# Optimization experiments

Measured on AMD Instinct MI355X. Metric: run time of the kernel, lower is better.

The kernel has to match this reference:

```python
import jax, jax.numpy as jnp
import numpy as np

B, S, D = 2, 2048, 4096
H, KVH, DH = 32, 8, 128
KVD = KVH * DH  # 1024
EPS = 1e-6
SCALING = DH ** -0.5


def _rms_norm(x, scale):
    xf = x.astype(jnp.float32)
    var = jnp.mean(xf * xf, axis=-1, keepdims=True)
    return (xf * jax.lax.rsqrt(var + EPS)).astype(x.dtype) * scale


def _rotate_half(x):
    half = x.shape[-1] // 2
    return jnp.concatenate([-x[..., half:], x[..., :half]], axis=-1)


def setup_inputs() -> dict:
    key = jax.random.key(0)
    ks = jax.random.split(key, 5)
    hidden_states = jax.random.normal(ks[0], (B, S, D), dtype=jnp.float32)
    w_qkv = jax.random.normal(ks[1], (D, D + 2 * KVD), dtype=jnp.float32) * 0.02
    w_out = jax.random.normal(ks[2], (D, D), dtype=jnp.float32) * 0.02
    q_scale = jnp.ones((D,), dtype=jnp.float32)
    k_scale = jnp.ones((KVD,), dtype=jnp.float32)
    # real rotary tables: cos/sin of positions, broadcast to batch
    inv_freq = 1.0 / (10000.0 ** (np.arange(0, DH, 2, dtype=np.float32) / DH))
    pos = np.arange(S, dtype=np.float32)
    freqs = np.outer(pos, inv_freq)            # [S, DH/2]
    emb = np.concatenate([freqs, freqs], -1)   # [S, DH]
    cos_cached = jnp.broadcast_to(jnp.asarray(np.cos(emb)), (B, S, DH))
    sin_cached = jnp.broadcast_to(jnp.asarray(np.sin(emb)), (B, S, DH))
    # causal mask: True = masked
    idx = jnp.arange(S)
    attention_mask = (idx[None, :] > idx[:, None])[None, None].repeat(B, 0)  # [B,1,S,S] bool
    return {
        "hidden_states": hidden_states, "w_qkv": w_qkv, "w_out": w_out,
        "q_scale": q_scale, "k_scale": k_scale,
        "cos_cached": cos_cached, "sin_cached": sin_cached,
        "attention_mask": attention_mask,
    }


def reference(hidden_states, w_qkv, w_out, q_scale, k_scale, cos_cached, sin_cached, attention_mask):
    b, s, _ = hidden_states.shape
    qkv = jnp.einsum("bsd,de->bse", hidden_states, w_qkv)
    q, k, v = jnp.split(qkv, [D, D + KVD], axis=-1)
    # qk-norm applied pre-view over full projected dim (non-qwen3 path)
    q = _rms_norm(q, q_scale)
    k = _rms_norm(k, k_scale)
    q = q.reshape(b, s, H, DH).transpose(0, 2, 1, 3)    # [B,H,S,DH]
    k = k.reshape(b, s, KVH, DH).transpose(0, 2, 1, 3)  # [B,KVH,S,DH]
    v = v.reshape(b, s, KVH, DH).transpose(0, 2, 1, 3)
    cos = cos_cached[:, None]  # [B,1,S,DH]
    sin = sin_cached[:, None]
    q = q * cos + _rotate_half(q) * sin
    k = k * cos + _rotate_half(k) * sin
    # repeat KV heads to match query heads (GQA)
    n_rep = H // KVH
    k = jnp.repeat(k, n_rep, axis=1)
    v = jnp.repeat(v, n_rep, axis=1)
    scores = jnp.einsum("bhsd,bhtd->bhst", q, k) * SCALING
    scores = jnp.where(attention_mask, jnp.float32(-10000.0), scores)
    attn = jax.nn.softmax(scores.astype(jnp.float32), axis=-1).astype(q.dtype)
    out = jnp.einsum("bhst,bhtd->bhsd", attn, v)
    out = out.transpose(0, 2, 1, 3).reshape(b, s, H * DH)
    return jnp.einsum("bsd,de->bse", out, w_out)
```

## Files before the change

kernel.cpp:

```cpp
#include <hip/hip_runtime.h>
#include <hip/hip_bf16.h>
#include <cstdint>
#include <cstddef>

#define BB 2
#define SS 2048
#define DD 4096
#define HH 32
#define KVH 8
#define DH 128
#define KVD 1024
#define SCALE 0.08838834764831845f
#define QSC 0.1275178745225f

typedef __attribute__((ext_vector_type(8))) short short8;
typedef __attribute__((ext_vector_type(4))) float f32x4;

typedef __attribute__((address_space(1))) void GV;
typedef __attribute__((address_space(3))) void LV;

__device__ __forceinline__ void async16(const void* g, void* l) {
  __builtin_amdgcn_global_load_lds((GV*)g, (LV*)l, 16, 0, 0);
}

__device__ __forceinline__ unsigned short f2bf(float x) {
  union { float f; uint32_t u; } v; v.f = x;
  uint32_t r = (v.u + 0x7fffu + ((v.u >> 16) & 1u)) >> 16;
  return (unsigned short)r;
}
__device__ __forceinline__ float bf2f(unsigned short b) {
  union { uint32_t u; float f; } v; v.u = ((uint32_t)b) << 16; return v.f;
}
__device__ __forceinline__ f32x4 mfma16(short8 a, short8 b, f32x4 c) {
  return __builtin_amdgcn_mfma_f32_16x16x32_bf16(a, b, c, 0, 0, 0);
}

__global__ __launch_bounds__(256) void cast_bf16_kernel(
    const float* __restrict__ in, unsigned short* __restrict__ out, int n4) {
  int i = blockIdx.x * 256 + threadIdx.x;
  if (i >= n4) return;
  float4 v = ((const float4*)in)[i];
  ushort4 o;
  o.x = f2bf(v.x); o.y = f2bf(v.y); o.z = f2bf(v.z); o.w = f2bf(v.w);
  ((ushort4*)out)[i] = o;
}

__global__ __launch_bounds__(256) void transpose_cast_kernel(
    const float* __restrict__ in, unsigned short* __restrict__ out, int R, int C) {
  __shared__ unsigned short tile[32][33];
  const int tx = threadIdx.x, ty = threadIdx.y;
  const int c0 = blockIdx.x * 32, r0 = blockIdx.y * 32;
  for (int i = ty; i < 32; i += 8)
    tile[i][tx] = f2bf(in[(size_t)(r0 + i) * C + c0 + tx]);
  __syncthreads();
  for (int i = ty; i < 32; i += 8)
    out[(size_t)(c0 + i) * R + r0 + tx] = tile[tx][i];
}

__global__ __launch_bounds__(256) void transpose_v_kernel(
    const unsigned short* __restrict__ qkv, unsigned short* __restrict__ vo) {
  __shared__ unsigned short tile[32][33];
  const int s0 = blockIdx.x * 32, d0 = blockIdx.y * 32;
  const int b = blockIdx.z >> 3, kvh = blockIdx.z & 7;
  const int tx = threadIdx.x, ty = threadIdx.y;
  const unsigned short* ip = qkv + 5120 + (size_t)kvh * 128 + d0 + tx;
  for (int i = ty; i < 32; i += 8)
    tile[i][tx] = ip[(size_t)(b * SS + s0 + i) * 6144];
  __syncthreads();
  unsigned short* op = vo + (size_t)(b * KVH + kvh) * DH * SS + s0 + tx;
  for (int i = ty; i < 32; i += 8)
    op[(size_t)(d0 + i) * SS] = tile[tx][i];
}

template <typename OutT>
__global__ __launch_bounds__(256, 2) void gemm_bt(
    const unsigned short* __restrict__ A, const unsigned short* __restrict__ Bt,
    OutT* __restrict__ C, int M, int N, int K) {
  __shared__ __align__(16) unsigned short As[4096];
  __shared__ __align__(16) unsigned short Bs[4096];
  const int tid = threadIdx.x;
  const int wave = tid >> 6, lane = tid & 63, quad = lane >> 4, l16 = lane & 15;
  const int m0 = blockIdx.x * 128, n0 = blockIdx.y * 128;
  const int wm = (wave & 1) * 64, wn = (wave >> 1) * 64;
  f32x4 acc[4][4] = {};
  const int sr = tid >> 2;
  const int sg = (tid & 3) ^ ((tid >> 3) & 3);
  const unsigned short* Ag = A + (size_t)(m0 + sr) * K + sg * 8;
  const unsigned short* Bg = Bt + (size_t)(n0 + sr) * K + sg * 8;
  unsigned short* AsW = As + wave * 512;
  unsigned short* BsW = Bs + wave * 512;
  const int pg = (quad ^ ((l16 >> 1) & 3)) * 8;
  for (int k0 = 0; k0 < K; k0 += 32) {
    __syncthreads();
    async16(Ag + k0, AsW);
    async16(Ag + (size_t)64 * K + k0, AsW + 2048);
    async16(Bg + k0, BsW);
    async16(Bg + (size_t)64 * K + k0, BsW + 2048);
    __syncthreads();
    short8 af[4], bf[4];
#pragma unroll
    for (int i = 0; i < 4; i++) {
      af[i] = *(const short8*)&As[(wm + i * 16 + l16) * 32 + pg];
      bf[i] = *(const short8*)&Bs[(wn + i * 16 + l16) * 32 + pg];
    }
#pragma unroll
    for (int mi = 0; mi < 4; mi++)
#pragma unroll
      for (int ni = 0; ni < 4; ni++)
        acc[mi][ni] = mfma16(af[mi], bf[ni], acc[mi][ni]);
  }
#pragma unroll
  for (int mi = 0; mi < 4; mi++)
#pragma unroll
    for (int ni = 0; ni < 4; ni++)
#pragma unroll
      for (int r = 0; r < 4; r++) {
        int row = m0 + wm + mi * 16 + quad * 4 + r;
        int col = n0 + wn + ni * 16 + l16;
        float v = acc[mi][ni][r];
        if constexpr (sizeof(OutT) == 4) C[(size_t)row * N + col] = v;
        else                             C[(size_t)row * N + col] = (OutT)f2bf(v);
      }
}

__global__ __launch_bounds__(256) void rmsnorm_rope_kernel(
    const unsigned short* __restrict__ qkv,
    const float* __restrict__ q_scale, const float* __restrict__ k_scale,
    const float* __restrict__ cosc, const float* __restrict__ sinc,
    unsigned short* __restrict__ qo,
    unsigned short* __restrict__ ko)
{
  const int row = blockIdx.x;
  const int b = row >> 11, s = row & 2047;
  const int tid = threadIdx.x;
  const unsigned short* qr = qkv + (size_t)row * 6144;
  short8 qv0 = *(const short8*)&qr[tid * 8];
  short8 qv1 = *(const short8*)&qr[2048 + tid * 8];
  ushort4 kv = *(const ushort4*)&qr[4096 + tid * 4];
  float sq = 0.f, sk = 0.f;
#pragma unroll
  for (int e = 0; e < 8; e++) {
    float a = bf2f((unsigned short)qv0[e]); sq += a * a;
    float c = bf2f((unsigned short)qv1[e]); sq += c * c;
  }
  float kf[4];
#pragma unroll
  for (int e = 0; e < 4; e++) {
    kf[e] = bf2f(((const unsigned short*)&kv)[e]); sk += kf[e] * kf[e];
  }
#pragma unroll
  for (int off = 32; off; off >>= 1) {
    sq += __shfl_down(sq, off, 64);
    sk += __shfl_down(sk, off, 64);
  }
  __shared__ float redq[4], redk[4];
  if ((tid & 63) == 0) { redq[tid >> 6] = sq; redk[tid >> 6] = sk; }
  __syncthreads();
  sq = redq[0] + redq[1] + redq[2] + redq[3];
  sk = redk[0] + redk[1] + redk[2] + redk[3];
  const float rq = rsqrtf(sq * (1.f / 4096.f) + 1e-6f);
  const float rk = rsqrtf(sk * (1.f / 1024.f) + 1e-6f);
  const float* cp = cosc + (size_t)row * 128;
  const float* sp = sinc + (size_t)row * 128;
#pragma unroll
  for (int it = 0; it < 2; it++) {
    const int c = it * 2048 + tid * 8;
    const int d = c & 127, hh = c >> 7;
    short8 v8 = it ? qv1 : qv0;
    short8 p8 = *(const short8*)&qr[c ^ 64];
    const float sgn = (d < 64) ? -1.f : 1.f;
    ushort o8[8];
#pragma unroll
    for (int e = 0; e < 8; e++) {
      float v = bf2f((unsigned short)v8[e]) * rq * q_scale[c + e];
      float p = bf2f((unsigned short)p8[e]) * rq * q_scale[(c ^ 64) + e];
      o8[e] = f2bf((v * cp[d + e] + sgn * p * sp[d + e]) * QSC);
    }
    *(uint4*)&qo[((size_t)(b * HH + hh) * SS + s) * DH + d] = *(const uint4*)o8;
  }
  {
    const int c = tid * 4;
    const int d = c & 127, hh = c >> 7;
    ushort4 p4 = *(const ushort4*)&qr[4096 + (c ^ 64)];
    const float sgn = (d < 64) ? -1.f : 1.f;
    ushort o4[4];
#pragma unroll
    for (int e = 0; e < 4; e++) {
      float v = kf[e] * rk * k_scale[c + e];
      float p = bf2f(((const unsigned short*)&p4)[e]) * rk * k_scale[(c ^ 64) + e];
      o4[e] = f2bf(v * cp[d + e] + sgn * p * sp[d + e]);
    }
    *(uint2*)&ko[((size_t)(b * KVH + hh) * SS + s) * DH + d] = *(const uint2*)o4;
  }
}

__global__ __launch_bounds__(256, 2) void flash_attn(
    const unsigned short* __restrict__ Q,
    const unsigned short* __restrict__ Kr,
    const unsigned short* __restrict__ Vt,
    unsigned short* __restrict__ O)
{
  __shared__ __align__(16) unsigned short Ks[8192];
  __shared__ __align__(16) unsigned short Vs[8192];
  __shared__ __align__(16) unsigned int   Ps[4][1024];
  const int tid = threadIdx.x, wave = tid >> 6, lane = tid & 63;
  const int quad = lane >> 4, l16 = lane & 15;
  const int bh = blockIdx.x, b = bh >> 5, h = bh & 31;
  const int kvh = h >> 2;
  const int qbase = ((int)gridDim.y - 1 - (int)blockIdx.y) * 128;
  const unsigned short* Qb = Q + (size_t)(b * HH + h) * SS * DH;
  short8 qf[2][4];
#pragma unroll
  for (int mi = 0; mi < 2; mi++) {
    const unsigned short* Qp = Qb + (size_t)(qbase + mi * 64 + wave * 16 + l16) * DH + quad * 8;
#pragma unroll
    for (int c = 0; c < 4; c++) qf[mi][c] = *(const short8*)(Qp + c * 32);
  }
  const unsigned short* Kg = Kr + (size_t)(b * KVH + kvh) * SS * DH;
  const unsigned short* Vg = Vt + (size_t)(b * KVH + kvh) * DH * SS;
  int bK[4], bV[4];
#pragma unroll
  for (int j = 0; j < 4; j++) {
    const int kk = wave * 16 + j * 4 + quad;
    const int gd = l16 ^ ((j * 4 + quad) & 15);
    bK[j] = kk * 128 + gd * 8;
    const int dd = (wave * 4 + j) * 8 + (lane >> 3);
    const int gk = (lane & 7) ^ ((lane >> 3) & 7);
    bV[j] = dd * 2048 + gk * 8;
  }
  f32x4 o[2][8] = {};
  float m_i[2] = {-1e30f, -1e30f}, l_i[2] = {0.f, 0.f};
  const int ndiag = qbase >> 6;
  const int nkt = ndiag + 2;
  for (int kt = 0; kt < nkt; kt++) {
    const int k0 = kt * 64;
    __syncthreads();
#pragma unroll
    for (int j = 0; j < 4; j++) {
      async16(Kg + (size_t)k0 * 128 + bK[j], Ks + (wave * 4 + j) * 512);
      async16(Vg + k0 + bV[j], Vs + (wave * 4 + j) * 512);
    }
    __syncthreads();
    f32x4 st[4][2] = {};
#pragma unroll
    for (int km = 0; km < 4; km++) {
      const unsigned short* krow = Ks + (km * 16 + l16) * 128;
#pragma unroll
      for (int c = 0; c < 4; c++) {
        short8 kf = *(const short8*)(krow + (((c * 4 + quad) ^ l16) * 8));
        st[km][0] = mfma16(kf, qf[0][c], st[km][0]);
        st[km][1] = mfma16(kf, qf[1][c], st[km][1]);
      }
    }
    const bool mtile = (kt >= ndiag);
    float alpha[2];
#pragma unroll
    for (int mi = 0; mi < 2; mi++) {
      if (mtile) {
        const int qg = qbase + mi * 64 + wave * 16 + l16;
#pragma unroll
        for (int km = 0; km < 4; km++)
#pragma unroll
          for (int r = 0; r < 4; r++)
            if (k0 + km * 16 + quad * 4 + r > qg) st[km][mi][r] = -1e4f;
      }
      float tmax = -3e38f;
#pragma unroll
      for (int km = 0; km < 4; km++)
#pragma unroll
        for (int r = 0; r < 4; r++) tmax = fmaxf(tmax, st[km][mi][r]);
      tmax = fmaxf(tmax, __shfl_xor(tmax, 16, 64));
      tmax = fmaxf(tmax, __shfl_xor(tmax, 32, 64));
      const float mn = fmaxf(m_i[mi], tmax);
      alpha[mi] = __builtin_amdgcn_exp2f(m_i[mi] - mn);
      m_i[mi] = mn;
      float rs = 0.f;
#pragma unroll
      for (int km = 0; km < 4; km++)
#pragma unroll
        for (int r = 0; r < 4; r++) {
          float e = __builtin_amdgcn_exp2f(st[km][mi][r] - mn);
          st[km][mi][r] = e;
          rs += e;
        }
      rs += __shfl_xor(rs, 16, 64);
      rs += __shfl_xor(rs, 32, 64);
      l_i[mi] = l_i[mi] * alpha[mi] + rs;
      unsigned int* pw = &Ps[wave][(mi * 16 + l16) * 32 + (quad & 1) * 2];
#pragma unroll
      for (int km = 0; km < 4; km++) {
        const int g = (km * 2 + (quad >> 1)) ^ (l16 & 7);
        float e0 = st[km][mi][0], e1 = st[km][mi][1], e2 = st[km][mi][2], e3 = st[km][mi][3];
        pw[g * 4]     = __builtin_amdgcn_perm(__builtin_bit_cast(unsigned int, e1),
                                              __builtin_bit_cast(unsigned int, e0), 0x07060302u);
        pw[g * 4 + 1] = __builtin_amdgcn_perm(__builtin_bit_cast(unsigned int, e3),
                                              __builtin_bit_cast(unsigned int, e2), 0x07060302u);
      }
    }
    if (__any((alpha[0] != 1.f) || (alpha[1] != 1.f))) {
#pragma unroll
      for (int mi = 0; mi < 2; mi++) {
        float ar[4];
#pragma unroll
        for (int r = 0; r < 4; r++)
          ar[r] = __shfl(alpha[mi], (lane & 48) + quad * 4 + r, 64);
#pragma unroll
        for (int f = 0; f < 8; f++)
#pragma unroll
          for (int r = 0; r < 4; r++) o[mi][f][r] *= ar[r];
      }
    }
#pragma unroll
    for (int kc = 0; kc < 2; kc++) {
      short8 pa[2];
#pragma unroll
      for (int mi = 0; mi < 2; mi++) {
        const int g = (kc * 4 + quad) ^ (l16 & 7);
        uint4 pv4 = *(const uint4*)&Ps[wave][(mi * 16 + l16) * 32 + g * 4];
        pa[mi] = __builtin_bit_cast(short8, pv4);
      }
#pragma unroll
      for (int f = 0; f < 8; f++) {
        const int d = f * 16 + l16;
        short8 vf = *(const short8*)(Vs + d * 64 + (((kc * 4 + quad) ^ (l16 & 7)) * 8));
        o[0][f] = mfma16(pa[0], vf, o[0][f]);
        o[1][f] = mfma16(pa[1], vf, o[1][f]);
      }
    }
  }
  float il[2][4];
#pragma unroll
  for (int mi = 0; mi < 2; mi++)
#pragma unroll
    for (int r = 0; r < 4; r++) {
      float lv = __shfl(l_i[mi], (lane & 48) + quad * 4 + r, 64);
      il[mi][r] = 1.f / lv;
    }
#pragma unroll
  for (int mi = 0; mi < 2; mi++) {
    unsigned short* Op = O + (size_t)(b * SS + qbase + mi * 64 + wave * 16 + quad * 4) * DD + h * DH + l16;
#pragma unroll
    for (int f = 0; f < 8; f++)
#pragma unroll
      for (int r = 0; r < 4; r++)
        Op[(size_t)r * DD + f * 16] = f2bf(o[mi][f][r] * il[mi][r]);
  }
}

extern "C" void kernel_launch(void* const* d_in, const int* in_sizes, int n_in,
                              void* d_out, int out_size, void* d_ws, size_t ws_size,
                              hipStream_t stream) {
  const float* hs      = (const float*)d_in[0];
  const float* wqkv    = (const float*)d_in[1];
  const float* wout    = (const float*)d_in[2];
  const float* q_scale = (const float*)d_in[3];
  const float* k_scale = (const float*)d_in[4];
  const float* cosc    = (const float*)d_in[5];
  const float* sinc    = (const float*)d_in[6];
  float* out = (float*)d_out;

  unsigned short* ws = (unsigned short*)d_ws;
  unsigned short* wqkvT = ws;
  unsigned short* woutT = wqkvT + 25165824;
  unsigned short* hsb   = woutT + 16777216;
  unsigned short* qkv   = hsb + 16777216;
  unsigned short* qrope = wqkvT;
  unsigned short* krope = wqkvT + 16777216;
  unsigned short* vT    = wqkvT + 16777216 + 4194304;
  unsigned short* attno = hsb;

  cast_bf16_kernel<<<16384, 256, 0, stream>>>(hs, hsb, 4194304);
  transpose_cast_kernel<<<dim3(192, 128), dim3(32, 8), 0, stream>>>(wqkv, wqkvT, 4096, 6144);
  transpose_cast_kernel<<<dim3(128, 128), dim3(32, 8), 0, stream>>>(wout, woutT, 4096, 4096);
  gemm_bt<unsigned short><<<dim3(32, 48), 256, 0, stream>>>(hsb, wqkvT, qkv, 4096, 6144, 4096);
  rmsnorm_rope_kernel<<<4096, 256, 0, stream>>>(qkv, q_scale, k_scale, cosc, sinc,
                                                qrope, krope);
  transpose_v_kernel<<<dim3(64, 4, 16), dim3(32, 8), 0, stream>>>(qkv, vT);
  flash_attn<<<dim3(64, 16), 256, 0, stream>>>(qrope, krope, vT, attno);
  gemm_bt<float><<<dim3(32, 32), 256, 0, stream>>>(attno, woutT, out, 4096, 4096, 4096);
}
```

Baseline: 800.2 us.

## Rewrite bf16 GEMM as 256x256 double-buffered ping-pong kernel with XCD-aware tile mapping

Replaces the 128x128, single-buffered GEMM (256 threads, K-step 32) with a 512-thread 256x256 tile kernel that uses K-step 64. It double-buffers LDS with async global-to-LDS loads issued two tiles ahead and splits each iteration into four MFMA phases separated by barriers and setprio hints. Block indices are remapped so consecutive tiles land on the same XCD for L2 reuse, and the LDS layout uses an XOR swizzle. The goal is to raise MFMA utilisation and hide global latency in both projection GEMMs. The cost is 128KB of LDS per block and a large accumulator register footprint. The 256-wide tiles also leave fewer blocks (384 and 256) to fill the CUs.

```diff
diff --git a/kernel.cpp b/kernel.cpp
--- a/kernel.cpp
+++ b/kernel.cpp
@@ -72,56 +72,180 @@
     op[(size_t)(d0 + i) * SS] = tile[tx][i];
 }
 
+
+#define GBAR()  asm volatile("s_barrier" ::: "memory")
+#define GLGKM0()                                              \
+  do {                                                        \
+    asm volatile("s_waitcnt lgkmcnt(0)" ::: "memory");        \
+    __builtin_amdgcn_sched_barrier(0);                        \
+  } while (0)
+
+#define STG_A(tt, mh, p)                                                         \
+  do {                                                                           \
+    async16(Abase + (size_t)(arb0 + (mh) * 64) * K + (size_t)(tt) * 64 + loffA,  \
+            ldsA + (p) * 16384 + (arb0 + (mh) * 64) * 64);                       \
+    async16(Abase + (size_t)(arb1 + (mh) * 64) * K + (size_t)(tt) * 64 + loffA,  \
+            ldsA + (p) * 16384 + (arb1 + (mh) * 64) * 64);                       \
+  } while (0)
+#define STG_B(tt, nh, p)                                                         \
+  do {                                                                           \
+    async16(Bbase + (size_t)(brb0 + (nh) * 32) * K + (size_t)(tt) * 64 + loffB,  \
+            ldsB + (p) * 16384 + (brb0 + (nh) * 32) * 64);                       \
+    async16(Bbase + (size_t)(brb1 + (nh) * 32) * K + (size_t)(tt) * 64 + loffB,  \
+            ldsB + (p) * 16384 + (brb1 + (nh) * 32) * 64);                       \
+  } while (0)
+
 template <typename OutT>
-__global__ __launch_bounds__(256, 2) void gemm_bt(
+__global__ __launch_bounds__(512, 2) void gemm_bt(
     const unsigned short* __restrict__ A, const unsigned short* __restrict__ Bt,
     OutT* __restrict__ C, int M, int N, int K) {
-  __shared__ __align__(16) unsigned short As[4096];
-  __shared__ __align__(16) unsigned short Bs[4096];
+  __shared__ __align__(16) unsigned short lds[65536];
+  unsigned short* ldsA = lds;
+  unsigned short* ldsB = lds + 32768;
   const int tid = threadIdx.x;
-  const int wave = tid >> 6, lane = tid & 63, quad = lane >> 4, l16 = lane & 15;
-  const int m0 = blockIdx.x * 128, n0 = blockIdx.y * 128;
-  const int wm = (wave & 1) * 64, wn = (wave >> 1) * 64;
-  f32x4 acc[4][4] = {};
-  const int sr = tid >> 2;
-  const int sg = (tid & 3) ^ ((tid >> 3) & 3);
-  const unsigned short* Ag = A + (size_t)(m0 + sr) * K + sg * 8;
-  const unsigned short* Bg = Bt + (size_t)(n0 + sr) * K + sg * 8;
-  unsigned short* AsW = As + wave * 512;
-  unsigned short* BsW = Bs + wave * 512;
-  const int pg = (quad ^ ((l16 >> 1) & 3)) * 8;
-  for (int k0 = 0; k0 < K; k0 += 32) {
-    __syncthreads();
-    async16(Ag + k0, AsW);
-    async16(Ag + (size_t)64 * K + k0, AsW + 2048);
-    async16(Bg + k0, BsW);
-    async16(Bg + (size_t)64 * K + k0, BsW + 2048);
-    __syncthreads();
-    short8 af[4], bf[4];
-#pragma unroll
-    for (int i = 0; i < 4; i++) {
-      af[i] = *(const short8*)&As[(wm + i * 16 + l16) * 32 + pg];
-      bf[i] = *(const short8*)&Bs[(wn + i * 16 + l16) * 32 + pg];
-    }
-#pragma unroll
-    for (int mi = 0; mi < 4; mi++)
-#pragma unroll
-      for (int ni = 0; ni < 4; ni++)
-        acc[mi][ni] = mfma16(af[mi], bf[ni], acc[mi][ni]);
-  }
-#pragma unroll
-  for (int mi = 0; mi < 4; mi++)
-#pragma unroll
-    for (int ni = 0; ni < 4; ni++)
-#pragma unroll
-      for (int r = 0; r < 4; r++) {
-        int row = m0 + wm + mi * 16 + quad * 4 + r;
-        int col = n0 + wn + ni * 16 + l16;
-        float v = acc[mi][ni][r];
-        if constexpr (sizeof(OutT) == 4) C[(size_t)row * N + col] = v;
-        else                             C[(size_t)row * N + col] = (OutT)f2bf(v);
-      }
-}
+  const int wave = __builtin_amdgcn_readfirstlane(tid >> 6);
+  const int lane = tid & 63, quad = lane >> 4, l16 = lane & 15;
+
+  const int tn_n = N >> 8;
+  const int nwg = (int)gridDim.x;
+  const int q = nwg >> 3, r = nwg & 7;
+  const int xcd = (int)blockIdx.x & 7, lin = (int)blockIdx.x >> 3;
+  const int wg = (xcd < r) ? xcd * (q + 1) + lin
+                           : r * (q + 1) + (xcd - r) * q + lin;
+  const int m0 = (wg / tn_n) * 256, n0 = (wg % tn_n) * 256;
+
+  const int blk0 = wave * 2, blk1 = blk0 + 1;
+  const int arb0 = ((blk0 & 7) << 3) + ((blk0 >> 3) << 7);
+  const int arb1 = ((blk1 & 7) << 3) + ((blk1 >> 3) << 7);
+  const int brb0 = ((blk0 >> 2) << 6) + ((blk0 & 3) << 3);
+  const int brb1 = ((blk1 >> 2) << 6) + ((blk1 & 3) << 3);
+  const int lrow = lane >> 3;
+  const int loffA = lrow * K + (((lane & 7) ^ lrow) << 3);
+  const int loffB = loffA;
+  const unsigned short* Abase = A + (size_t)m0 * K;
+  const unsigned short* Bbase = Bt + (size_t)n0 * K;
+
+  const int pg0 = ((quad) ^ (l16 & 7)) * 8;
+  const int pg1 = ((quad + 4) ^ (l16 & 7)) * 8;
+  const int arow = ((wave >> 2) * 128 + l16) * 64;
+  const int brow = ((wave & 3) * 64 + l16) * 64;
+
+  f32x4 acc[8][4] = {};
+  short8 a0[4], a1[4], bl0[2], bl1[2], bh0[2], bh1[2];
+
+  STG_A(0, 0, 0); STG_B(0, 0, 0); STG_B(0, 1, 0); STG_A(0, 1, 0);
+  STG_A(1, 0, 1); STG_B(1, 0, 1); STG_B(1, 1, 1); STG_A(1, 1, 1);
+  asm volatile("s_waitcnt vmcnt(8)" ::: "memory");
+  GBAR();
+
+  const int nt = K >> 6;
+  for (int t = 0; t < nt; ++t) {
+    const int p = t & 1;
+    const bool st = (t + 2 < nt);
+    const unsigned short* pA = ldsA + p * 16384 + arow;
+    const unsigned short* pB = ldsB + p * 16384 + brow;
+
+#pragma unroll
+    for (int i = 0; i < 4; ++i) {
+      a0[i] = *(const short8*)(pA + i * 1024 + pg0);
+      a1[i] = *(const short8*)(pA + i * 1024 + pg1);
+    }
+#pragma unroll
+    for (int j = 0; j < 2; ++j) {
+      bl0[j] = *(const short8*)(pB + j * 1024 + pg0);
+      bl1[j] = *(const short8*)(pB + j * 1024 + pg1);
+    }
+    GBAR();
+    GLGKM0();
+    __builtin_amdgcn_s_setprio(1);
+#pragma unroll
+    for (int i = 0; i < 4; ++i)
+#pragma unroll
+      for (int j = 0; j < 2; ++j) {
+        acc[i][j] = mfma16(a0[i], bl0[j], acc[i][j]);
+        acc[i][j] = mfma16(a1[i], bl1[j], acc[i][j]);
+      }
+    __builtin_amdgcn_sched_barrier(0);
+    __builtin_amdgcn_s_setprio(0);
+    GBAR();
+
+#pragma unroll
+    for (int j = 0; j < 2; ++j) {
+      bh0[j] = *(const short8*)(pB + (j + 2) * 1024 + pg0);
+      bh1[j] = *(const short8*)(pB + (j + 2) * 1024 + pg1);
+    }
+    if (st) STG_A(t + 2, 0, p);
+    GBAR();
+    GLGKM0();
+    __builtin_amdgcn_s_setprio(1);
+#pragma unroll
+    for (int i = 0; i < 4; ++i)
+#pragma unroll
+      for (int j = 0; j < 2; ++j) {
+        acc[i][j + 2] = mfma16(a0[i], bh0[j], acc[i][j + 2]);
+        acc[i][j + 2] = mfma16(a1[i], bh1[j], acc[i][j + 2]);
+      }
+    __builtin_amdgcn_sched_barrier(0);
+    __builtin_amdgcn_s_setprio(0);
+    GBAR();
+
+#pragma unroll
+    for (int i = 0; i < 4; ++i) {
+      a0[i] = *(const short8*)(pA + (i + 4) * 1024 + pg0);
+      a1[i] = *(const short8*)(pA + (i + 4) * 1024 + pg1);
+    }
+    if (st) STG_B(t + 2, 0, p);
+    GBAR();
+    GLGKM0();
+    __builtin_amdgcn_s_setprio(1);
+#pragma unroll
+    for (int i = 0; i < 4; ++i)
+#pragma unroll
+      for (int j = 0; j < 2; ++j) {
+        acc[i + 4][j + 2] = mfma16(a0[i], bh0[j], acc[i + 4][j + 2]);
+        acc[i + 4][j + 2] = mfma16(a1[i], bh1[j], acc[i + 4][j + 2]);
+      }
+    __builtin_amdgcn_sched_barrier(0);
+    __builtin_amdgcn_s_setprio(0);
+    GBAR();
+
+    if (st) {
+      STG_B(t + 2, 1, p);
+      STG_A(t + 2, 1, p);
+      asm volatile("s_waitcnt vmcnt(8)" ::: "memory");
+    } else {
+      asm volatile("s_waitcnt vmcnt(0)" ::: "memory");
+    }
+    GBAR();
+    __builtin_amdgcn_s_setprio(1);
+#pragma unroll
+    for (int i = 0; i < 4; ++i)
+#pragma unroll
+      for (int j = 0; j < 2; ++j) {
+        acc[i + 4][j] = mfma16(a0[i], bl0[j], acc[i + 4][j]);
+        acc[i + 4][j] = mfma16(a1[i], bl1[j], acc[i + 4][j]);
+      }
+    __builtin_amdgcn_sched_barrier(0);
+    __builtin_amdgcn_s_setprio(0);
+    GBAR();
+  }
+
+  const int cm = m0 + (wave >> 2) * 128 + quad * 4;
+  const int cn = n0 + (wave & 3) * 64 + l16;
+#pragma unroll
+  for (int i = 0; i < 8; ++i)
+#pragma unroll
+    for (int j = 0; j < 4; ++j)
+#pragma unroll
+      for (int rr = 0; rr < 4; ++rr) {
+        const size_t idx = (size_t)(cm + i * 16 + rr) * N + (cn + j * 16);
+        if constexpr (sizeof(OutT) == 4) C[idx] = acc[i][j][rr];
+        else                             C[idx] = (OutT)f2bf(acc[i][j][rr]);
+      }
+}
+
+#undef STG_A
+#undef STG_B
 
 __global__ __launch_bounds__(256) void rmsnorm_rope_kernel(
     const unsigned short* __restrict__ qkv,
@@ -372,10 +496,10 @@
   cast_bf16_kernel<<<16384, 256, 0, stream>>>(hs, hsb, 4194304);
   transpose_cast_kernel<<<dim3(192, 128), dim3(32, 8), 0, stream>>>(wqkv, wqkvT, 4096, 6144);
   transpose_cast_kernel<<<dim3(128, 128), dim3(32, 8), 0, stream>>>(wout, woutT, 4096, 4096);
-  gemm_bt<unsigned short><<<dim3(32, 48), 256, 0, stream>>>(hsb, wqkvT, qkv, 4096, 6144, 4096);
+  gemm_bt<unsigned short><<<dim3(384), 512, 0, stream>>>(hsb, wqkvT, qkv, 4096, 6144, 4096);
   rmsnorm_rope_kernel<<<4096, 256, 0, stream>>>(qkv, q_scale, k_scale, cosc, sinc,
                                                 qrope, krope);
   transpose_v_kernel<<<dim3(64, 4, 16), dim3(32, 8), 0, stream>>>(qkv, vT);
   flash_attn<<<dim3(64, 16), 256, 0, stream>>>(qrope, krope, vT, attno);
-  gemm_bt<float><<<dim3(32, 32), 256, 0, stream>>>(attno, woutT, out, 4096, 4096, 4096);
-}
+  gemm_bt<float><<<dim3(256), 512, 0, stream>>>(attno, woutT, out, 4096, 4096, 4096);
+}
```

After: 752.4 us. -6.0%, faster.
